# Performance work log

Hardware: AMD Instinct MI355X
Metric: run time of the kernel (lower is better)

Reference implementation:

```python
import jax, jax.numpy as jnp
import numpy as np

B = 4096   # batch
V = 512    # num_variables
H = 64     # hidden_dim


def setup_inputs() -> dict:
    key = jax.random.key(0)
    ks = jax.random.split(key, 6)
    return {
        "X": jax.random.normal(ks[0], (B, V), dtype=jnp.float32),
        "adjacency_logits": jax.random.normal(ks[1], (V, V), dtype=jnp.float32) * 0.1,
        # W1[i] is the first Linear of net i: maps V inputs -> H hidden
        "W1": jax.random.normal(ks[2], (V, V, H), dtype=jnp.float32) * (1.0 / np.sqrt(V)),
        "b1": jax.random.normal(ks[3], (V, H), dtype=jnp.float32) * 0.01,
        # W2[i] is the second Linear of net i: maps H hidden -> 1 output
        "W2": jax.random.normal(ks[4], (V, H), dtype=jnp.float32) * (1.0 / np.sqrt(H)),
        "b2": jax.random.normal(ks[5], (V,), dtype=jnp.float32) * 0.01,
    }


def reference(X, adjacency_logits, W1, b1, W2, b2):
    # Hard adjacency (hard_adjacency=True path): threshold sigmoid, zero diagonal.
    probs = jax.nn.sigmoid(adjacency_logits)
    adj = (probs > 0.5).astype(X.dtype) * (1.0 - jnp.eye(V, dtype=X.dtype))  # [V, V]

    # Original loop: for each i, net_i(X * adj[:, i]).
    # Fold the parent mask into the first-layer weights: W1_eff[i, v, h] = W1[i, v, h] * adj[v, i]
    W1_eff = W1 * adj.T[:, :, None]                      # [V, V, H]
    h = jax.nn.relu(jnp.einsum('bv,ivh->bih', X, W1_eff) + b1[None])  # [B, V, H]
    reconstructed = jnp.einsum('bih,ih->bi', h, W2) + b2[None]        # [B, V]
    return reconstructed, adj
```

## Files before the change

### kernel.cpp

```cpp
#include <hip/hip_runtime.h>
#include <hip/hip_bf16.h>
#include <stdint.h>

#define BB 4096
#define VV 512
#define HH 64

typedef short bf16x8 __attribute__((ext_vector_type(8)));
typedef float floatx4 __attribute__((ext_vector_type(4)));
typedef unsigned short ushort8 __attribute__((ext_vector_type(8)));

typedef const __attribute__((address_space(1))) void g_void;
typedef __attribute__((address_space(3))) void l_void;

__device__ __forceinline__ void gload_lds16(const void* g, void* l) {
    __builtin_amdgcn_global_load_lds((g_void*)g, (l_void*)l, 16, 0, 0);
}

__device__ __forceinline__ unsigned short f2bf_rne(float f) {
    unsigned int u = __float_as_uint(f);
    u += 0x7FFFu + ((u >> 16) & 1u);
    return (unsigned short)(u >> 16);
}

__global__ __launch_bounds__(256) void adj_kernel(const float* __restrict__ logits,
                                                  float* __restrict__ adj_out) {
    int idx = blockIdx.x * 256 + threadIdx.x;
    int v = idx >> 9, u = idx & (VV - 1);
    adj_out[idx] = (logits[idx] > 0.0f && v != u) ? 1.0f : 0.0f;
}

__global__ __launch_bounds__(256) void prep_fused_kernel(
        const float* __restrict__ X, const float* __restrict__ logits,
        const float* __restrict__ W1, float* __restrict__ adj_out,
        unsigned short* __restrict__ Xp, unsigned short* __restrict__ W1t) {
    __shared__ float tile[64][65];
    __shared__ float maskv[64];
    int bx = blockIdx.x;
    int t  = threadIdx.x;
    if (bx < 4096) {
        int i  = bx >> 3;
        int v0 = (bx & 7) << 6;
        if (t < 64) {
            int v = v0 + t;
            maskv[t] = (logits[(size_t)v * VV + i] > 0.0f && v != i) ? 1.0f : 0.0f;
        }
        const float4* src4 = (const float4*)(W1 + ((size_t)i * VV + v0) * HH);
        #pragma unroll
        for (int jj = 0; jj < 4; ++jj) {
            int c  = jj * 256 + t;
            int vr = c >> 4, h4 = c & 15;
            float4 w = src4[c];
            tile[vr][h4 * 4 + 0] = w.x;
            tile[vr][h4 * 4 + 1] = w.y;
            tile[vr][h4 * 4 + 2] = w.z;
            tile[vr][h4 * 4 + 3] = w.w;
        }
        __syncthreads();
        unsigned short* dst = W1t + (size_t)i * (HH * VV) + v0;
        #pragma unroll
        for (int j = 0; j < 2; ++j) {
            int c = j * 256 + t;
            int h = c >> 3;
            int vr0 = (c & 7) * 8;
            ushort8 o;
            #pragma unroll
            for (int r = 0; r < 8; ++r)
                o[r] = f2bf_rne(tile[vr0 + r][h] * maskv[vr0 + r]);
            *(ushort8*)&dst[(size_t)h * VV + vr0] = o;
        }
    } else {
        int idx = (bx - 4096) * 256 + t;
        {
            int v = idx >> 9, u = idx & (VV - 1);
            adj_out[idx] = (logits[idx] > 0.0f && v != u) ? 1.0f : 0.0f;
        }
        {
            int lane = idx & 63;
            int mt   = (idx >> 6) & 3;
            int ks   = (idx >> 8) & 15;
            int rb   = idx >> 12;
            int row  = rb * 64 + mt * 16 + (lane & 15);
            int k0   = ks * 32 + (lane >> 4) * 8;
            const float4* s4 = (const float4*)(X + (size_t)row * VV + k0);
            float4 a = s4[0], b = s4[1];
            ushort8 o;
            o[0] = f2bf_rne(a.x); o[1] = f2bf_rne(a.y);
            o[2] = f2bf_rne(a.z); o[3] = f2bf_rne(a.w);
            o[4] = f2bf_rne(b.x); o[5] = f2bf_rne(b.y);
            o[6] = f2bf_rne(b.z); o[7] = f2bf_rne(b.w);
            *(ushort8*)(Xp + (size_t)idx * 8) = o;
        }
    }
}

__global__ __launch_bounds__(256, 3) void dag_gemm_kernel(
        const unsigned short* __restrict__ Xp,
        const unsigned short* __restrict__ W1t,
        const float* __restrict__ b1,
        const float* __restrict__ W2,
        const float* __restrict__ b2,
        float* __restrict__ outT)
{
    __shared__ __align__(16) unsigned short Ws[16384];
    __shared__ float Po[256];

    const int t    = threadIdx.x;
    const int wave = t >> 6;
    const int lane = t & 63;
    const int ln   = lane & 15;
    const int quad = lane >> 4;

    const int bx   = blockIdx.x;
    const int i    = bx >> 4;
    const int row0 = (bx & 15) << 8;

    auto ldb = [&](int pos, int nt) -> bf16x8 {
        return *(const bf16x8*)&Ws[(nt * 16 + ln) * 256 + ((pos ^ (ln & 7)) * 8)];
    };

    const unsigned short* abase =
        Xp + (size_t)((row0 >> 6) + wave) * (64 * VV) + lane * 8;

    bf16x8 af[4][4];
    #pragma unroll
    for (int s = 0; s < 3; ++s)
        #pragma unroll
        for (int mt = 0; mt < 4; ++mt)
            af[s][mt] = *(const bf16x8*)(abase + (s * 4 + mt) * 512);

    const unsigned short* wbase = W1t + (size_t)i * (HH * VV);
    #pragma unroll
    for (int j = 0; j < 8; ++j) {
        int c = j * 256 + t;
        int h = c >> 5, s2 = c & 31;
        gload_lds16(wbase + (size_t)h * VV + (size_t)(s2 ^ (h & 7)) * 8,
                    (char*)Ws + c * 16);
    }
    __syncthreads();

    floatx4 acc[4][4];
    #pragma unroll
    for (int a = 0; a < 4; ++a)
        #pragma unroll
        for (int b = 0; b < 4; ++b)
            acc[a][b] = (floatx4){0.f, 0.f, 0.f, 0.f};

    bf16x8 bq[2][4];
    #pragma unroll
    for (int nt = 0; nt < 4; ++nt)
        bq[0][nt] = ldb(quad, nt);

    #pragma unroll
    for (int kk = 0; kk < 8; ++kk) {
        #pragma unroll
        for (int mt = 0; mt < 4; ++mt)
            af[(kk + 3) & 3][mt] =
                *(const bf16x8*)(abase + ((kk + 3) * 4 + mt) * 512);
        if (kk < 7) {
            #pragma unroll
            for (int nt = 0; nt < 4; ++nt)
                bq[(kk + 1) & 1][nt] = ldb((kk + 1) * 4 + quad, nt);
        }
        #pragma unroll
        for (int mt = 0; mt < 4; ++mt)
            #pragma unroll
            for (int nt = 0; nt < 4; ++nt)
                acc[mt][nt] = __builtin_amdgcn_mfma_f32_16x16x32_bf16(
                    af[kk & 3][mt], bq[kk & 1][nt], acc[mt][nt], 0, 0, 0);
    }

    __syncthreads();

    #pragma unroll
    for (int j = 0; j < 8; ++j) {
        int c = j * 256 + t;
        int h = c >> 5, s2 = c & 31;
        gload_lds16(wbase + (size_t)h * VV + (size_t)(32 + (s2 ^ (h & 7))) * 8,
                    (char*)Ws + c * 16);
    }
    __syncthreads();

    #pragma unroll
    for (int nt = 0; nt < 4; ++nt)
        bq[0][nt] = ldb(quad, nt);

    #pragma unroll
    for (int kk = 8; kk < 16; ++kk) {
        if (kk < 13) {
            #pragma unroll
            for (int mt = 0; mt < 4; ++mt)
                af[(kk + 3) & 3][mt] =
                    *(const bf16x8*)(abase + ((kk + 3) * 4 + mt) * 512);
        }
        if (kk < 15) {
            #pragma unroll
            for (int nt = 0; nt < 4; ++nt)
                bq[(kk + 1) & 1][nt] = ldb(((kk + 1) - 8) * 4 + quad, nt);
        }
        #pragma unroll
        for (int mt = 0; mt < 4; ++mt)
            #pragma unroll
            for (int nt = 0; nt < 4; ++nt)
                acc[mt][nt] = __builtin_amdgcn_mfma_f32_16x16x32_bf16(
                    af[kk & 3][mt], bq[kk & 1][nt], acc[mt][nt], 0, 0, 0);
    }

    float b1v[4], w2v[4];
    #pragma unroll
    for (int nt = 0; nt < 4; ++nt) {
        b1v[nt] = b1[i * HH + nt * 16 + ln];
        w2v[nt] = W2[i * HH + nt * 16 + ln];
    }
    const float b2i = b2[i];
    #pragma unroll
    for (int mt = 0; mt < 4; ++mt) {
        #pragma unroll
        for (int r = 0; r < 4; ++r) {
            float p = 0.f;
            #pragma unroll
            for (int nt = 0; nt < 4; ++nt) {
                float hv = acc[mt][nt][r] + b1v[nt];
                hv = hv > 0.f ? hv : 0.f;
                p += hv * w2v[nt];
            }
            p += __shfl_xor(p, 8);
            p += __shfl_xor(p, 4);
            p += __shfl_xor(p, 2);
            p += __shfl_xor(p, 1);
            if (ln == 0)
                Po[wave * 64 + mt * 16 + quad * 4 + r] = p + b2i;
        }
    }
    outT[(size_t)i * BB + row0 + wave * 64 + lane] = Po[wave * 64 + lane];
}

__global__ __launch_bounds__(256) void transpose_kernel(const float* __restrict__ outT,
                                                        float* __restrict__ out) {
    __shared__ float tile[64][65];
    int i0 = (blockIdx.x & 7) * 64;
    int r0 = (blockIdx.x >> 3) * 64;
    int t  = threadIdx.x;
    #pragma unroll
    for (int j = 0; j < 16; ++j) {
        int idx = j * 256 + t;
        int ii = idx >> 6, rr = idx & 63;
        tile[ii][rr] = outT[(size_t)(i0 + ii) * BB + r0 + rr];
    }
    __syncthreads();
    #pragma unroll
    for (int j = 0; j < 16; ++j) {
        int idx = j * 256 + t;
        int rr = idx >> 6, ii = idx & 63;
        out[(size_t)(r0 + rr) * VV + i0 + ii] = tile[ii][rr];
    }
}

__global__ __launch_bounds__(256) void fallback_kernel(
        const float* __restrict__ X, const float* __restrict__ logits,
        const float* __restrict__ W1, const float* __restrict__ b1,
        const float* __restrict__ W2, const float* __restrict__ b2,
        float* __restrict__ out) {
    __shared__ float Wc[128][64];
    int i   = blockIdx.x & (VV - 1);
    int row = (blockIdx.x >> 9) * 256 + threadIdx.x;
    float acc[64];
    #pragma unroll
    for (int h = 0; h < 64; ++h) acc[h] = 0.f;
    for (int v0 = 0; v0 < VV; v0 += 128) {
        __syncthreads();
        for (int j = 0; j < 32; ++j) {
            int idx = j * 256 + threadIdx.x;
            int vr = idx >> 6, h = idx & 63;
            int v = v0 + vr;
            float m = (logits[(size_t)v * VV + i] > 0.f && v != i) ? 1.f : 0.f;
            Wc[vr][h] = W1[((size_t)i * VV + v) * HH + h] * m;
        }
        __syncthreads();
        for (int vr = 0; vr < 128; ++vr) {
            float xv = X[(size_t)row * VV + v0 + vr];
            #pragma unroll
            for (int h = 0; h < 64; ++h) acc[h] += xv * Wc[vr][h];
        }
    }
    float p = b2[i];
    #pragma unroll
    for (int h = 0; h < 64; ++h) {
        float hv = acc[h] + b1[i * HH + h];
        p += (hv > 0.f ? hv : 0.f) * W2[i * HH + h];
    }
    out[(size_t)row * VV + i] = p;
}

extern "C" void kernel_launch(void* const* d_in, const int* in_sizes, int n_in,
                              void* d_out, int out_size, void* d_ws, size_t ws_size,
                              hipStream_t stream) {
    const float* X      = (const float*)d_in[0];
    const float* logits = (const float*)d_in[1];
    const float* W1     = (const float*)d_in[2];
    const float* b1     = (const float*)d_in[3];
    const float* W2     = (const float*)d_in[4];
    const float* b2     = (const float*)d_in[5];

    float* out     = (float*)d_out;
    float* adj_out = out + (size_t)BB * VV;

    const size_t xp_bytes   = (size_t)BB * VV * 2;
    const size_t w1t_bytes  = (size_t)VV * HH * VV * 2;
    const size_t outt_bytes = (size_t)BB * VV * 4;
    const size_t need = xp_bytes + w1t_bytes + outt_bytes;

    if (ws_size >= need) {
        unsigned short* Xp   = (unsigned short*)d_ws;
        unsigned short* W1t  = (unsigned short*)((char*)d_ws + xp_bytes);
        float*          outT = (float*)((char*)d_ws + xp_bytes + w1t_bytes);
        hipLaunchKernelGGL(prep_fused_kernel, dim3(5120), dim3(256), 0, stream,
                           X, logits, W1, adj_out, Xp, W1t);
        hipLaunchKernelGGL(dag_gemm_kernel, dim3(8192), dim3(256), 0, stream,
                           Xp, W1t, b1, W2, b2, outT);
        hipLaunchKernelGGL(transpose_kernel, dim3((BB / 64) * (VV / 64)), dim3(256), 0, stream,
                           outT, out);
    } else {
        hipLaunchKernelGGL(adj_kernel, dim3((VV * VV) / 256), dim3(256), 0, stream,
                           logits, adj_out);
        hipLaunchKernelGGL(fallback_kernel, dim3(VV * (BB / 256)), dim3(256), 0, stream,
                           X, logits, W1, b1, W2, b2, out);
    }
}
```

Baseline: 253.9 us.

## Retile DAG GEMM to 256x256 blocks with triple-buffered LDS staging for A and B

Each GEMM block now computes 256 batch rows for four networks with 512 threads, so every staged tile of X is reused across four networks instead of one. Both X and W1 tiles go through global_load_lds into a three-stage LDS ring with swizzled layout, explicit waitcnt/barrier pipelining, and setprio around the MFMA bursts. X is now stored row-major in bf16, with no pre-packed fragment layout. The gain is less redundant X traffic and better overlap of loads with compute, at the cost of much more LDS, more accumulator registers per thread, and tight hand-written synchronisation.

```diff
diff --git a/kernel.cpp b/kernel.cpp
--- a/kernel.cpp
+++ b/kernel.cpp
@@ -33,7 +33,7 @@
 __global__ __launch_bounds__(256) void prep_fused_kernel(
         const float* __restrict__ X, const float* __restrict__ logits,
         const float* __restrict__ W1, float* __restrict__ adj_out,
-        unsigned short* __restrict__ Xp, unsigned short* __restrict__ W1t) {
+        unsigned short* __restrict__ Xb, unsigned short* __restrict__ W1t) {
     __shared__ float tile[64][65];
     __shared__ float maskv[64];
     int bx = blockIdx.x;
@@ -76,136 +76,127 @@
             adj_out[idx] = (logits[idx] > 0.0f && v != u) ? 1.0f : 0.0f;
         }
         {
-            int lane = idx & 63;
-            int mt   = (idx >> 6) & 3;
-            int ks   = (idx >> 8) & 15;
-            int rb   = idx >> 12;
-            int row  = rb * 64 + mt * 16 + (lane & 15);
-            int k0   = ks * 32 + (lane >> 4) * 8;
-            const float4* s4 = (const float4*)(X + (size_t)row * VV + k0);
+            const float4* s4 = (const float4*)(X + (size_t)idx * 8);
             float4 a = s4[0], b = s4[1];
             ushort8 o;
             o[0] = f2bf_rne(a.x); o[1] = f2bf_rne(a.y);
             o[2] = f2bf_rne(a.z); o[3] = f2bf_rne(a.w);
             o[4] = f2bf_rne(b.x); o[5] = f2bf_rne(b.y);
             o[6] = f2bf_rne(b.z); o[7] = f2bf_rne(b.w);
-            *(ushort8*)(Xp + (size_t)idx * 8) = o;
-        }
-    }
-}
-
-__global__ __launch_bounds__(256, 3) void dag_gemm_kernel(
-        const unsigned short* __restrict__ Xp,
+            *(ushort8*)(Xb + (size_t)idx * 8) = o;
+        }
+    }
+}
+
+__global__ __launch_bounds__(512, 2) void dag_gemm_kernel(
+        const unsigned short* __restrict__ Xb,
         const unsigned short* __restrict__ W1t,
         const float* __restrict__ b1,
         const float* __restrict__ W2,
         const float* __restrict__ b2,
         float* __restrict__ outT)
 {
-    __shared__ __align__(16) unsigned short Ws[16384];
-    __shared__ float Po[256];
-
-    const int t    = threadIdx.x;
-    const int wave = t >> 6;
-    const int lane = t & 63;
+    __shared__ __align__(16) unsigned short As[3 * 8192];
+    __shared__ __align__(16) unsigned short Bs[3 * 8192];
+    __shared__ float Po[1024];
+
+    const int tid  = threadIdx.x;
+    const int wave = tid >> 6;
+    const int lane = tid & 63;
     const int ln   = lane & 15;
     const int quad = lane >> 4;
+    const int wr   = wave >> 2;
+    const int wn   = wave & 3;
 
     const int bx   = blockIdx.x;
-    const int i    = bx >> 4;
-    const int row0 = (bx & 15) << 8;
-
-    auto ldb = [&](int pos, int nt) -> bf16x8 {
-        return *(const bf16x8*)&Ws[(nt * 16 + ln) * 256 + ((pos ^ (ln & 7)) * 8)];
+    const int ig   = ((bx & 7) << 4) + ((bx >> 3) & 15);
+    const int m    = bx >> 7;
+    const int i0   = ig << 2;
+    const int row0 = m << 8;
+
+    const int rA = tid >> 2, jc = tid & 3, sw = (tid >> 3) & 3;
+    const unsigned short* srcA = Xb + (size_t)(row0 + rA) * VV + ((jc ^ sw) << 3);
+    const unsigned short* srcB = W1t + (size_t)(i0 + (rA >> 6)) * (HH * VV)
+                                     + (size_t)(rA & 63) * VV + ((jc ^ sw) << 3);
+    char* dstA = (char*)As + (tid << 4);
+    char* dstB = (char*)Bs + (tid << 4);
+
+    auto stageA = [&](int t, int buf) {
+        gload_lds16(srcA + t * 32,         dstA + (buf << 14));
+        gload_lds16(srcA + t * 32 + 65536, dstA + (buf << 14) + 8192);
     };
-
-    const unsigned short* abase =
-        Xp + (size_t)((row0 >> 6) + wave) * (64 * VV) + lane * 8;
-
-    bf16x8 af[4][4];
-    #pragma unroll
-    for (int s = 0; s < 3; ++s)
-        #pragma unroll
-        for (int mt = 0; mt < 4; ++mt)
-            af[s][mt] = *(const bf16x8*)(abase + (s * 4 + mt) * 512);
-
-    const unsigned short* wbase = W1t + (size_t)i * (HH * VV);
-    #pragma unroll
-    for (int j = 0; j < 8; ++j) {
-        int c = j * 256 + t;
-        int h = c >> 5, s2 = c & 31;
-        gload_lds16(wbase + (size_t)h * VV + (size_t)(s2 ^ (h & 7)) * 8,
-                    (char*)Ws + c * 16);
-    }
-    __syncthreads();
-
-    floatx4 acc[4][4];
-    #pragma unroll
-    for (int a = 0; a < 4; ++a)
+    auto stageB = [&](int t, int buf) {
+        gload_lds16(srcB + t * 32,         dstB + (buf << 14));
+        gload_lds16(srcB + t * 32 + 65536, dstB + (buf << 14) + 8192);
+    };
+
+    const int slot = (quad ^ ((ln >> 1) & 3)) << 4;
+    const int aoff = (((wr << 7) + ln) << 6) + slot;
+    const int boff = (((wn << 6) + ln) << 6) + slot;
+
+    floatx4 acc[8][4];
+    #pragma unroll
+    for (int a = 0; a < 8; ++a)
         #pragma unroll
         for (int b = 0; b < 4; ++b)
             acc[a][b] = (floatx4){0.f, 0.f, 0.f, 0.f};
 
-    bf16x8 bq[2][4];
-    #pragma unroll
-    for (int nt = 0; nt < 4; ++nt)
-        bq[0][nt] = ldb(quad, nt);
-
-    #pragma unroll
-    for (int kk = 0; kk < 8; ++kk) {
+    stageA(0, 0); stageB(0, 0); stageA(1, 1); stageB(1, 1);
+    asm volatile("s_waitcnt vmcnt(4)" ::: "memory");
+    asm volatile("s_barrier" ::: "memory");
+
+    bf16x8 af[8], bq[4];
+    #pragma unroll
+    for (int t = 0; t < 16; ++t) {
+        const int buf  = t % 3;
+        const int nbuf = (t + 2) % 3;
+        const char* ab = (const char*)As + (buf << 14);
+        const char* bb = (const char*)Bs + (buf << 14);
+
         #pragma unroll
         for (int mt = 0; mt < 4; ++mt)
-            af[(kk + 3) & 3][mt] =
-                *(const bf16x8*)(abase + ((kk + 3) * 4 + mt) * 512);
-        if (kk < 7) {
-            #pragma unroll
-            for (int nt = 0; nt < 4; ++nt)
-                bq[(kk + 1) & 1][nt] = ldb((kk + 1) * 4 + quad, nt);
-        }
+            af[mt] = *(const bf16x8*)(ab + aoff + (mt << 10));
+        #pragma unroll
+        for (int nt = 0; nt < 4; ++nt)
+            bq[nt] = *(const bf16x8*)(bb + boff + (nt << 10));
+        if (t <= 13) stageA(t + 2, nbuf);
+        asm volatile("s_barrier" ::: "memory");
+        asm volatile("s_waitcnt lgkmcnt(0)" ::: "memory");
+        __builtin_amdgcn_sched_barrier(0);
+        __builtin_amdgcn_s_setprio(1);
         #pragma unroll
         for (int mt = 0; mt < 4; ++mt)
             #pragma unroll
             for (int nt = 0; nt < 4; ++nt)
                 acc[mt][nt] = __builtin_amdgcn_mfma_f32_16x16x32_bf16(
-                    af[kk & 3][mt], bq[kk & 1][nt], acc[mt][nt], 0, 0, 0);
-    }
-
-    __syncthreads();
-
-    #pragma unroll
-    for (int j = 0; j < 8; ++j) {
-        int c = j * 256 + t;
-        int h = c >> 5, s2 = c & 31;
-        gload_lds16(wbase + (size_t)h * VV + (size_t)(32 + (s2 ^ (h & 7))) * 8,
-                    (char*)Ws + c * 16);
-    }
-    __syncthreads();
-
-    #pragma unroll
-    for (int nt = 0; nt < 4; ++nt)
-        bq[0][nt] = ldb(quad, nt);
-
-    #pragma unroll
-    for (int kk = 8; kk < 16; ++kk) {
-        if (kk < 13) {
-            #pragma unroll
-            for (int mt = 0; mt < 4; ++mt)
-                af[(kk + 3) & 3][mt] =
-                    *(const bf16x8*)(abase + ((kk + 3) * 4 + mt) * 512);
-        }
-        if (kk < 15) {
-            #pragma unroll
-            for (int nt = 0; nt < 4; ++nt)
-                bq[(kk + 1) & 1][nt] = ldb(((kk + 1) - 8) * 4 + quad, nt);
-        }
-        #pragma unroll
-        for (int mt = 0; mt < 4; ++mt)
+                    af[mt], bq[nt], acc[mt][nt], 0, 0, 0);
+        __builtin_amdgcn_s_setprio(0);
+        asm volatile("s_barrier" ::: "memory");
+
+        #pragma unroll
+        for (int mt = 4; mt < 8; ++mt)
+            af[mt] = *(const bf16x8*)(ab + aoff + (mt << 10));
+        if (t <= 13) stageB(t + 2, nbuf);
+        asm volatile("s_barrier" ::: "memory");
+        asm volatile("s_waitcnt lgkmcnt(0)" ::: "memory");
+        __builtin_amdgcn_sched_barrier(0);
+        __builtin_amdgcn_s_setprio(1);
+        #pragma unroll
+        for (int mt = 4; mt < 8; ++mt)
             #pragma unroll
             for (int nt = 0; nt < 4; ++nt)
                 acc[mt][nt] = __builtin_amdgcn_mfma_f32_16x16x32_bf16(
-                    af[kk & 3][mt], bq[kk & 1][nt], acc[mt][nt], 0, 0, 0);
-    }
-
+                    af[mt], bq[nt], acc[mt][nt], 0, 0, 0);
+        __builtin_amdgcn_s_setprio(0);
+
+        if (t < 15) {
+            if (t <= 13) asm volatile("s_waitcnt vmcnt(4)" ::: "memory");
+            else         asm volatile("s_waitcnt vmcnt(0)" ::: "memory");
+            asm volatile("s_barrier" ::: "memory");
+        }
+    }
+
+    const int i = i0 + wn;
     float b1v[4], w2v[4];
     #pragma unroll
     for (int nt = 0; nt < 4; ++nt) {
@@ -214,7 +205,7 @@
     }
     const float b2i = b2[i];
     #pragma unroll
-    for (int mt = 0; mt < 4; ++mt) {
+    for (int mt = 0; mt < 8; ++mt) {
         #pragma unroll
         for (int r = 0; r < 4; ++r) {
             float p = 0.f;
@@ -229,10 +220,15 @@
             p += __shfl_xor(p, 2);
             p += __shfl_xor(p, 1);
             if (ln == 0)
-                Po[wave * 64 + mt * 16 + quad * 4 + r] = p + b2i;
-        }
-    }
-    outT[(size_t)i * BB + row0 + wave * 64 + lane] = Po[wave * 64 + lane];
+                Po[(wn << 8) + (wr << 7) + mt * 16 + (quad << 2) + r] = p + b2i;
+        }
+    }
+    __syncthreads();
+    {
+        int il = tid >> 7, rr = (tid & 127) << 1;
+        *(float2*)&outT[(size_t)(i0 + il) * BB + row0 + rr] =
+            *(const float2*)&Po[(il << 8) + rr];
+    }
 }
 
 __global__ __launch_bounds__(256) void transpose_kernel(const float* __restrict__ outT,
@@ -305,19 +301,19 @@
     float* out     = (float*)d_out;
     float* adj_out = out + (size_t)BB * VV;
 
-    const size_t xp_bytes   = (size_t)BB * VV * 2;
+    const size_t xb_bytes   = (size_t)BB * VV * 2;
     const size_t w1t_bytes  = (size_t)VV * HH * VV * 2;
     const size_t outt_bytes = (size_t)BB * VV * 4;
-    const size_t need = xp_bytes + w1t_bytes + outt_bytes;
+    const size_t need = xb_bytes + w1t_bytes + outt_bytes;
 
     if (ws_size >= need) {
-        unsigned short* Xp   = (unsigned short*)d_ws;
-        unsigned short* W1t  = (unsigned short*)((char*)d_ws + xp_bytes);
-        float*          outT = (float*)((char*)d_ws + xp_bytes + w1t_bytes);
+        unsigned short* Xb   = (unsigned short*)d_ws;
+        unsigned short* W1t  = (unsigned short*)((char*)d_ws + xb_bytes);
+        float*          outT = (float*)((char*)d_ws + xb_bytes + w1t_bytes);
         hipLaunchKernelGGL(prep_fused_kernel, dim3(5120), dim3(256), 0, stream,
-                           X, logits, W1, adj_out, Xp, W1t);
-        hipLaunchKernelGGL(dag_gemm_kernel, dim3(8192), dim3(256), 0, stream,
-                           Xp, W1t, b1, W2, b2, outT);
+                           X, logits, W1, adj_out, Xb, W1t);
+        hipLaunchKernelGGL(dag_gemm_kernel, dim3(2048), dim3(512), 0, stream,
+                           Xb, W1t, b1, W2, b2, outT);
         hipLaunchKernelGGL(transpose_kernel, dim3((BB / 64) * (VV / 64)), dim3(256), 0, stream,
                            outT, out);
     } else {
```

New measurement: 271.8 us. 7.0% more time.

## Write GEMM output directly to final layout and drop transpose kernel

Applied to the files above, without the earlier changes.

The GEMM kernel now writes each result straight into the row-major [B,V] output instead of a transposed staging buffer, which removes the separate transpose kernel launch and the extra 8 MB round trip through the workspace. Block indices are remapped so that consecutive blocks are spread across the 8 XCDs by net index, letting blocks that share an i-range write neighbouring output columns. The direct stores are strided by V (one float per row per block), so write coalescing gets worse in exchange for removing a kernel launch and a full read-and-write pass.

```diff
diff --git a/kernel.cpp b/kernel.cpp
--- a/kernel.cpp
+++ b/kernel.cpp
@@ -100,7 +100,7 @@
         const float* __restrict__ b1,
         const float* __restrict__ W2,
         const float* __restrict__ b2,
-        float* __restrict__ outT)
+        float* __restrict__ out)
 {
     __shared__ __align__(16) unsigned short Ws[16384];
     __shared__ float Po[256];
@@ -111,9 +111,10 @@
     const int ln   = lane & 15;
     const int quad = lane >> 4;
 
-    const int bx   = blockIdx.x;
-    const int i    = bx >> 4;
-    const int row0 = (bx & 15) << 8;
+    const int bx    = blockIdx.x;
+    const int local = bx >> 3;
+    const int i     = ((bx & 7) << 6) + (local >> 4);
+    const int row0  = (local & 15) << 8;
 
     auto ldb = [&](int pos, int nt) -> bf16x8 {
         return *(const bf16x8*)&Ws[(nt * 16 + ln) * 256 + ((pos ^ (ln & 7)) * 8)];
@@ -232,28 +233,7 @@
                 Po[wave * 64 + mt * 16 + quad * 4 + r] = p + b2i;
         }
     }
-    outT[(size_t)i * BB + row0 + wave * 64 + lane] = Po[wave * 64 + lane];
-}
-
-__global__ __launch_bounds__(256) void transpose_kernel(const float* __restrict__ outT,
-                                                        float* __restrict__ out) {
-    __shared__ float tile[64][65];
-    int i0 = (blockIdx.x & 7) * 64;
-    int r0 = (blockIdx.x >> 3) * 64;
-    int t  = threadIdx.x;
-    #pragma unroll
-    for (int j = 0; j < 16; ++j) {
-        int idx = j * 256 + t;
-        int ii = idx >> 6, rr = idx & 63;
-        tile[ii][rr] = outT[(size_t)(i0 + ii) * BB + r0 + rr];
-    }
-    __syncthreads();
-    #pragma unroll
-    for (int j = 0; j < 16; ++j) {
-        int idx = j * 256 + t;
-        int rr = idx >> 6, ii = idx & 63;
-        out[(size_t)(r0 + rr) * VV + i0 + ii] = tile[ii][rr];
-    }
+    out[(size_t)(row0 + wave * 64 + lane) * VV + i] = Po[wave * 64 + lane];
 }
 
 __global__ __launch_bounds__(256) void fallback_kernel(
@@ -305,21 +285,17 @@
     float* out     = (float*)d_out;
     float* adj_out = out + (size_t)BB * VV;
 
-    const size_t xp_bytes   = (size_t)BB * VV * 2;
-    const size_t w1t_bytes  = (size_t)VV * HH * VV * 2;
-    const size_t outt_bytes = (size_t)BB * VV * 4;
-    const size_t need = xp_bytes + w1t_bytes + outt_bytes;
+    const size_t xp_bytes  = (size_t)BB * VV * 2;
+    const size_t w1t_bytes = (size_t)VV * HH * VV * 2;
+    const size_t need = xp_bytes + w1t_bytes;
 
     if (ws_size >= need) {
-        unsigned short* Xp   = (unsigned short*)d_ws;
-        unsigned short* W1t  = (unsigned short*)((char*)d_ws + xp_bytes);
-        float*          outT = (float*)((char*)d_ws + xp_bytes + w1t_bytes);
+        unsigned short* Xp  = (unsigned short*)d_ws;
+        unsigned short* W1t = (unsigned short*)((char*)d_ws + xp_bytes);
         hipLaunchKernelGGL(prep_fused_kernel, dim3(5120), dim3(256), 0, stream,
                            X, logits, W1, adj_out, Xp, W1t);
         hipLaunchKernelGGL(dag_gemm_kernel, dim3(8192), dim3(256), 0, stream,
-                           Xp, W1t, b1, W2, b2, outT);
-        hipLaunchKernelGGL(transpose_kernel, dim3((BB / 64) * (VV / 64)), dim3(256), 0, stream,
-                           outT, out);
+                           Xp, W1t, b1, W2, b2, out);
     } else {
         hipLaunchKernelGGL(adj_kernel, dim3((VV * VV) / 256), dim3(256), 0, stream,
                            logits, adj_out);
```

New measurement: 256.7 us. No clear change (+1.1%).
